# Optimization experiments

Hardware: AMD Instinct MI355X
Metric: run time of the kernel (lower is better)

## Reference

```python
import jax, jax.numpy as jnp
import numpy as np

B, S, C, HEADS = 1, 4096, 640, 8
AH, AW = 64, 64            # attn-resolution grid, AH*AW == S
MH, MW = 512, 512          # full-res mask size
NEG = -1e9                 # finite large negative (safe for fully-masked rows)


def nearest_resize(x, h, w):
    # torch F.interpolate(mode='nearest'): idx = floor(i * H_in / H_out)
    H, W = x.shape[-2], x.shape[-1]
    ri = (jnp.arange(h) * H) // h
    ci = (jnp.arange(w) * W) // w
    return x[..., ri, :][..., :, ci]


def sdpa(q, k, v, mask, heads):
    # q,k,v: [B,S,C]; mask: [B,1,S,S] bool (True = attend), broadcasts over heads
    b, s, c = q.shape
    d = c // heads
    qh = q.reshape(b, s, heads, d).transpose(0, 2, 1, 3)  # bhsd
    kh = k.reshape(b, s, heads, d).transpose(0, 2, 1, 3)
    vh = v.reshape(b, s, heads, d).transpose(0, 2, 1, 3)
    scores = jnp.einsum('bhqd,bhkd->bhqk', qh, kh) / jnp.sqrt(jnp.asarray(d, qh.dtype))
    scores = jnp.where(mask, scores, NEG)
    attn = jax.nn.softmax(scores, axis=-1)
    out = jnp.einsum('bhqk,bhkd->bhqd', attn, vh)
    return out.transpose(0, 2, 1, 3).reshape(b, s, c)


def setup_inputs():
    key = jax.random.key(0)
    ks = jax.random.split(key, 14)
    std = 1.0 / np.sqrt(C)
    w = lambda k: (jax.random.normal(k, (C, C), jnp.float32) * std)
    return {
        'hidden_states': jax.random.normal(ks[0], (B, S, C), jnp.float32),
        'mask': jax.random.randint(ks[1], (B, 1, MH, MW), 0, 4, jnp.int32),
        'inpainting_mask': jax.random.randint(ks[2], (B, 1, MH, MW), 0, 2, jnp.int32),
        'Wq': w(ks[3]), 'Wk': w(ks[4]), 'Wv': w(ks[5]),
        'Wq_ent': w(ks[6]), 'Wk_ent': w(ks[7]), 'Wv_ent': w(ks[8]),
        'Wq_out': w(ks[9]), 'Wk_out': w(ks[10]), 'Wv_out': w(ks[11]),
        'Wo': w(ks[12]),
    }


def reference(hidden_states, mask, inpainting_mask, Wq, Wk, Wv,
              Wq_ent, Wk_ent, Wv_ent, Wq_out, Wk_out, Wv_out, Wo):
    residual = hidden_states
    b, s, c = hidden_states.shape

    # --- interpolation-derived masks (kept as [B,1,S,S]; broadcasts over heads) ---
    m = nearest_resize(mask, AH, AW).reshape(b, 1, s)                 # entity labels
    attn_mask = m[:, :, :, None] == m[:, :, None, :]                  # same-entity [B,1,S,S]
    im = nearest_resize(inpainting_mask, AH, AW).reshape(b, 1, s)
    outside_key = (im[:, :, None, :] == 0)                            # [B,1,1,S]
    attn_mask_outside = attn_mask & outside_key                       # [B,1,S,S]

    # --- projections ---
    q = hidden_states @ Wq.T
    k = hidden_states @ Wk.T
    v = hidden_states @ Wv.T
    q_e = hidden_states @ Wq_ent.T
    k_e = hidden_states @ Wk_ent.T
    v_e = hidden_states @ Wv_ent.T
    q_o = hidden_states @ Wq_out.T
    k_o = hidden_states @ Wk_out.T
    v_o = hidden_states @ Wv_out.T

    # --- three SDPA branches ---
    hs_orig = sdpa(q, k, v, attn_mask, HEADS)            # original attention
    hs_ent = sdpa(q_e, k_e, v_e, attn_mask, 1)           # entity attention (1 head)
    hs_out = sdpa(q_o, k_o, v_o, attn_mask_outside, HEADS)  # outside attention

    hs = hs_orig + hs_ent + hs_out
    return hs @ Wo.T + residual
```

## Files before the change

kernel.cpp:

```cpp
#include <hip/hip_runtime.h>
#include <cstdint>

typedef __attribute__((ext_vector_type(8))) short bf16x8;
typedef __attribute__((ext_vector_type(4))) short bf16x4;
typedef __attribute__((ext_vector_type(4))) float f32x4;

#define S_LEN 4096
#define CDIM  640
#define NPROJ 5760

__device__ __forceinline__ f32x4 mfma16(bf16x4 a, bf16x4 b, f32x4 c){
#if defined(__HIP_DEVICE_COMPILE__) && __HIP_DEVICE_COMPILE__
  return __builtin_amdgcn_mfma_f32_16x16x16bf16_1k(a, b, c, 0, 0, 0);
#else
  (void)a; (void)b;
  return c;
#endif
}

__device__ __forceinline__ void gload_lds(const unsigned short* g, unsigned short* l){
#if defined(__HIP_DEVICE_COMPILE__) && __HIP_DEVICE_COMPILE__
  __builtin_amdgcn_global_load_lds((const __attribute__((address_space(1))) unsigned int*)g,
                                   (__attribute__((address_space(3))) unsigned int*)l, 16, 0, 0);
#else
  (void)g; (void)l;
#endif
}

__device__ __forceinline__ unsigned short f2bf(float f){
  union { float f; uint32_t u; } v; v.f = f;
  uint32_t u = v.u;
  return (unsigned short)((u + 0x7fffu + ((u >> 16) & 1u)) >> 16);
}
__device__ __forceinline__ float b2f(unsigned short h){
  union { uint32_t u; float f; } v; v.u = ((uint32_t)h) << 16;
  return v.f;
}

__global__ void k_labels(const int* __restrict__ mask, const int* __restrict__ inp,
                         int* __restrict__ labels){
  int s = blockIdx.x * 256 + threadIdx.x;
  if (s >= S_LEN) return;
  int y = s >> 6, x = s & 63;
  int off = (y * 8) * 512 + x * 8;
  int m = mask[off] & 0xff;
  int o = (inp[off] == 0) ? 0x100 : 0;
  labels[s] = m | o;
}

__global__ void k_hist(const int* __restrict__ labels, int* __restrict__ boff, int* __restrict__ cnt){
  __shared__ int h[4];
  if (threadIdx.x < 4) h[threadIdx.x] = 0;
  __syncthreads();
  for (int s = threadIdx.x; s < S_LEN; s += 256) atomicAdd(&h[labels[s] & 3], 1);
  __syncthreads();
  if (threadIdx.x == 0){
    int a = 0;
    for (int c = 0; c < 4; c++){ boff[c] = a; a += h[c]; }
    boff[4] = a;
  }
  if (threadIdx.x < 4) cnt[threadIdx.x] = 0;
}

__global__ void k_perm(const int* __restrict__ labels, const int* __restrict__ boff,
                       int* __restrict__ cnt, int* __restrict__ perm,
                       int* __restrict__ inv, int* __restrict__ labP){
  int s = blockIdx.x * 256 + threadIdx.x;
  if (s >= S_LEN) return;
  int lab = labels[s];
  int c = lab & 3;
  int pos = boff[c] + atomicAdd(&cnt[c], 1);
  perm[pos] = s; inv[s] = pos; labP[pos] = lab;
}

__global__ void k_tiles(const int* __restrict__ labP, const int* __restrict__ boff,
                        int4* __restrict__ qtinfo, float* __restrict__ rowsum){
  int t = threadIdx.x;
  __shared__ int nkt[32];
  if (t < 32){
    int c0 = labP[t * 128] & 3, c1 = labP[t * 128 + 127] & 3;
    int lo = boff[c0] & ~127, hi = (boff[c1 + 1] + 127) & ~127;
    qtinfo[t].x = lo; qtinfo[t].y = hi; qtinfo[t].w = 0;
    nkt[t] = (hi - lo) >> 7;
  }
  __syncthreads();
  if (t == 0){
    int a = 0;
    for (int i = 0; i < 32; i++){ qtinfo[i].z = a; a += nkt[i]; }
  }
  for (int s = t; s < S_LEN; s += 256) rowsum[s] = 0.f;
}

__global__ void k_cvt_hs(const float* __restrict__ src, unsigned short* __restrict__ dst, int n){
  int idx = (blockIdx.x * 256 + threadIdx.x) * 4;
  if (idx >= n) return;
  float4 v = *(const float4*)(src + idx);
  ushort4 o;
  o.x = f2bf(v.x); o.y = f2bf(v.y); o.z = f2bf(v.z); o.w = f2bf(v.w);
  *(ushort4*)(dst + idx) = o;
}

struct WPtrs { const float* w[10]; };

__global__ void k_cvt_w(WPtrs p, unsigned short* __restrict__ dst){
  int e = (blockIdx.x * 256 + threadIdx.x) * 4;
  if (e >= 10 * 409600) return;
  int a = e / 409600, r = e % 409600;
  float sc = (a == 0 || a == 6) ? 0.11180339887498948f
           : (a == 3 ? 0.03952847075210474f : 1.0f);
  float4 v = *(const float4*)(p.w[a] + r);
  ushort4 o;
  o.x = f2bf(v.x * sc); o.y = f2bf(v.y * sc); o.z = f2bf(v.z * sc); o.w = f2bf(v.w * sc);
  *(ushort4*)(dst + e) = o;
}

template<int EPI>
__global__ __launch_bounds__(256) void k_gemm(const unsigned short* __restrict__ A,
                                              const unsigned short* __restrict__ B,
                                              int M, int N, int K, int ldc,
                                              const int* __restrict__ rowmap,
                                              unsigned short* __restrict__ Cb,
                                              float* __restrict__ Cf,
                                              const float* __restrict__ resid){
  __shared__ __align__(16) unsigned short As[128 * 32];
  __shared__ __align__(16) unsigned short Bs[128 * 32];
  int m0 = blockIdx.y * 128, n0 = blockIdx.x * 128;
  int tid = threadIdx.x;
  int wid = tid >> 6, lane = tid & 63;
  int quad = lane >> 4, l16 = lane & 15;
  int wm = (wid >> 1) * 64, wn = (wid & 1) * 64;
  f32x4 acc[4][4];
#pragma unroll
  for (int i = 0; i < 4; i++)
#pragma unroll
    for (int j = 0; j < 4; j++) acc[i][j] = f32x4{0.f, 0.f, 0.f, 0.f};

  for (int k0 = 0; k0 < K; k0 += 32){
    __syncthreads();
#pragma unroll
    for (int u = 0; u < 2; u++){
      int c = tid + u * 256;
      int row = c >> 2, off = (c & 3) * 8;
      gload_lds(&A[(size_t)(m0 + row) * K + k0 + off], &As[c * 8]);
      gload_lds(&B[(size_t)(n0 + row) * K + k0 + off], &Bs[c * 8]);
    }
    __syncthreads();
    bf16x8 af[4], bfr[4];
#pragma unroll
    for (int t = 0; t < 4; t++){
      af[t]  = *(const bf16x8*)(&As[(wm + t * 16 + l16) * 32 + quad * 8]);
      bfr[t] = *(const bf16x8*)(&Bs[(wn + t * 16 + l16) * 32 + quad * 8]);
    }
#pragma unroll
    for (int mt = 0; mt < 4; mt++)
#pragma unroll
      for (int nt = 0; nt < 4; nt++)
        acc[mt][nt] = __builtin_amdgcn_mfma_f32_16x16x32_bf16(af[mt], bfr[nt], acc[mt][nt], 0, 0, 0);
  }
#pragma unroll
  for (int mt = 0; mt < 4; mt++)
#pragma unroll
    for (int nt = 0; nt < 4; nt++)
#pragma unroll
      for (int r = 0; r < 4; r++){
        int row = m0 + wm + mt * 16 + quad * 4 + r;
        int col = n0 + wn + nt * 16 + l16;
        float v = acc[mt][nt][r];
        if (EPI == 0){
          Cb[(size_t)rowmap[row] * ldc + col] = f2bf(v);
        } else {
          int ro = rowmap[row];
          Cf[(size_t)ro * ldc + col] = v + resid[(size_t)ro * ldc + col];
        }
      }
}

__global__ void k_transpose_v(const unsigned short* __restrict__ proj, unsigned short* __restrict__ vT){
  __shared__ unsigned short T[64][65];
  int z = blockIdx.z;
  int s0 = blockIdx.x * 64, c0 = blockIdx.y * 64;
  int colbase = 1280 + z * 1920 + c0;
  unsigned short* dst = vT + (size_t)z * CDIM * S_LEN;
  int tid = threadIdx.x;
  for (int i = tid; i < 64 * 64; i += 256){
    int r = i >> 6, c = i & 63;
    T[r][c] = proj[(size_t)(s0 + r) * NPROJ + colbase + c];
  }
  __syncthreads();
  for (int i = tid; i < 64 * 64; i += 256){
    int c = i >> 6, r = i & 63;
    dst[(size_t)(c0 + c) * S_LEN + s0 + r] = T[r][c];
  }
}

#define KP 84
#define VP 76
__global__ __launch_bounds__(256, 2) void k_attn80(const unsigned short* __restrict__ proj,
                                                   const unsigned short* __restrict__ vT,
                                                   const int* __restrict__ labP,
                                                   const int4* __restrict__ qtinfo,
                                                   unsigned short* __restrict__ outP){
  __shared__ __align__(16) unsigned short Ks[64 * KP];
  __shared__ __align__(16) unsigned short Vt[80 * VP];
  __shared__ __align__(16) int labk[64];
  int tid = threadIdx.x, wid = tid >> 6, lane = tid & 63;
  int quad = lane >> 4, l16 = lane & 15;
  int q0 = blockIdx.x * 128;
  int h  = blockIdx.y;
  bool OUTSIDE = (blockIdx.z == 1);
  int qc = (OUTSIDE ? 3840 : 0) + h * 80;
  int kc = (OUTSIDE ? 4480 : 640) + h * 80;
  const unsigned short* vTb = vT + (size_t)(OUTSIDE ? 2 : 0) * CDIM * S_LEN;
  int4 qi = qtinfo[blockIdx.x];
  int t0 = qi.x >> 6, t1 = qi.y >> 6;

  int qrow0 = q0 + wid * 32 + l16;
  int qrow1 = qrow0 + 16;
  bf16x4 qf0[5], qf1[5];
#pragma unroll
  for (int dc = 0; dc < 5; dc++){
    qf0[dc] = *(const bf16x4*)&proj[(size_t)qrow0 * NPROJ + qc + dc * 16 + quad * 4];
    qf1[dc] = *(const bf16x4*)&proj[(size_t)qrow1 * NPROJ + qc + dc * 16 + quad * 4];
  }
  int lq0 = labP[qrow0] & 0xff, lq1 = labP[qrow1] & 0xff;

  float lp0 = 0.f, lp1 = 0.f;
  f32x4 Oc0[5], Oc1[5];
#pragma unroll
  for (int t = 0; t < 5; t++){ Oc0[t] = f32x4{0.f,0.f,0.f,0.f}; Oc1[t] = f32x4{0.f,0.f,0.f,0.f}; }

  for (int kt = t0; kt < t1; kt++){
    int key0 = kt * 64;
    __syncthreads();
#pragma unroll
    for (int u = 0; u < 3; u++){
      int c = tid + u * 256;
      if (c < 640){
        int krow = c / 10, koff = (c % 10) * 8;
        int vrow = c >> 3, voff = (c & 7) * 8;
        *(uint4*)&Ks[krow * KP + koff] =
          *(const uint4*)&proj[(size_t)(key0 + krow) * NPROJ + kc + koff];
        *(uint4*)&Vt[vrow * VP + voff] =
          *(const uint4*)&vTb[(size_t)(h * 80 + vrow) * S_LEN + key0 + voff];
      }
    }
    if (tid < 64) labk[tid] = labP[key0 + tid];
    __syncthreads();

#pragma unroll
    for (int kg = 0; kg < 4; kg++){
      f32x4 sa0 = f32x4{0.f,0.f,0.f,0.f}, sa1 = f32x4{0.f,0.f,0.f,0.f};
#pragma unroll
      for (int dc = 0; dc < 5; dc++){
        bf16x4 kf = *(const bf16x4*)&Ks[(kg * 16 + l16) * KP + dc * 16 + quad * 4];
        sa0 = mfma16(kf, qf0[dc], sa0);
        sa1 = mfma16(kf, qf1[dc], sa1);
      }
      int4 lk4 = *(const int4*)&labk[kg * 16 + quad * 4];
      bool m0 = !OUTSIDE || (lk4.x & 0x100), m1 = !OUTSIDE || (lk4.y & 0x100);
      bool m2 = !OUTSIDE || (lk4.z & 0x100), m3 = !OUTSIDE || (lk4.w & 0x100);
      int k0l = lk4.x & 0xff, k1l = lk4.y & 0xff, k2l = lk4.z & 0xff, k3l = lk4.w & 0xff;
      bf16x4 pf0, pf1;
      {
        float p0 = (k0l == lq0 && m0) ? __expf(sa0[0]) : 0.f;
        float p1 = (k1l == lq0 && m1) ? __expf(sa0[1]) : 0.f;
        float p2 = (k2l == lq0 && m2) ? __expf(sa0[2]) : 0.f;
        float p3 = (k3l == lq0 && m3) ? __expf(sa0[3]) : 0.f;
        lp0 += (p0 + p1) + (p2 + p3);
        pf0[0] = (short)f2bf(p0); pf0[1] = (short)f2bf(p1);
        pf0[2] = (short)f2bf(p2); pf0[3] = (short)f2bf(p3);
      }
      {
        float p0 = (k0l == lq1 && m0) ? __expf(sa1[0]) : 0.f;
        float p1 = (k1l == lq1 && m1) ? __expf(sa1[1]) : 0.f;
        float p2 = (k2l == lq1 && m2) ? __expf(sa1[2]) : 0.f;
        float p3 = (k3l == lq1 && m3) ? __expf(sa1[3]) : 0.f;
        lp1 += (p0 + p1) + (p2 + p3);
        pf1[0] = (short)f2bf(p0); pf1[1] = (short)f2bf(p1);
        pf1[2] = (short)f2bf(p2); pf1[3] = (short)f2bf(p3);
      }
#pragma unroll
      for (int dt = 0; dt < 5; dt++){
        bf16x4 vf = *(const bf16x4*)&Vt[(dt * 16 + l16) * VP + kg * 16 + quad * 4];
        Oc0[dt] = mfma16(vf, pf0, Oc0[dt]);
        Oc1[dt] = mfma16(vf, pf1, Oc1[dt]);
      }
    }
  }
  lp0 += __shfl_xor(lp0, 16); lp0 += __shfl_xor(lp0, 32);
  lp1 += __shfl_xor(lp1, 16); lp1 += __shfl_xor(lp1, 32);
  float iL0 = 1.f / lp0, iL1 = 1.f / lp1;
  unsigned short* dst = outP + (size_t)blockIdx.z * S_LEN * CDIM;
#pragma unroll
  for (int dt = 0; dt < 5; dt++){
    ushort4 o;
    o.x = f2bf(Oc0[dt][0] * iL0); o.y = f2bf(Oc0[dt][1] * iL0);
    o.z = f2bf(Oc0[dt][2] * iL0); o.w = f2bf(Oc0[dt][3] * iL0);
    *(ushort4*)&dst[(size_t)qrow0 * CDIM + h * 80 + dt * 16 + quad * 4] = o;
    o.x = f2bf(Oc1[dt][0] * iL1); o.y = f2bf(Oc1[dt][1] * iL1);
    o.z = f2bf(Oc1[dt][2] * iL1); o.w = f2bf(Oc1[dt][3] * iL1);
    *(ushort4*)&dst[(size_t)qrow1 * CDIM + h * 80 + dt * 16 + quad * 4] = o;
  }
}

__global__ __launch_bounds__(256) void k_ent_qk(const unsigned short* __restrict__ proj,
                                                const int* __restrict__ labP,
                                                const int4* __restrict__ qtinfo,
                                                unsigned short* __restrict__ Sbuf,
                                                float* __restrict__ rowsum){
  int qt = blockIdx.y;
  int4 qi = qtinfo[qt];
  int nkt = (qi.y - qi.x) >> 7;
  if ((int)blockIdx.x >= nkt) return;
  int m0 = qt * 128, n0 = qi.x + blockIdx.x * 128;
  __shared__ __align__(16) unsigned short As[128 * 32];
  __shared__ __align__(16) unsigned short Bs[128 * 32];
  __shared__ int lQ[128], lK[128];
  int tid = threadIdx.x, wid = tid >> 6, lane = tid & 63;
  int quad = lane >> 4, l16 = lane & 15;
  int wm = (wid >> 1) * 64, wn = (wid & 1) * 64;
  if (tid < 128) lQ[tid] = labP[m0 + tid] & 0xff;
  else           lK[tid - 128] = labP[n0 + tid - 128] & 0xff;
  f32x4 acc[4][4];
#pragma unroll
  for (int i = 0; i < 4; i++)
#pragma unroll
    for (int j = 0; j < 4; j++) acc[i][j] = f32x4{0.f, 0.f, 0.f, 0.f};

  for (int k0 = 0; k0 < 640; k0 += 32){
    __syncthreads();
#pragma unroll
    for (int u = 0; u < 2; u++){
      int c = tid + u * 256;
      int row = c >> 2, off = (c & 3) * 8;
      gload_lds(&proj[(size_t)(m0 + row) * NPROJ + 1920 + k0 + off], &As[c * 8]);
      gload_lds(&proj[(size_t)(n0 + row) * NPROJ + 2560 + k0 + off], &Bs[c * 8]);
    }
    __syncthreads();
    bf16x8 af[4], bfr[4];
#pragma unroll
    for (int t = 0; t < 4; t++){
      af[t]  = *(const bf16x8*)(&As[(wm + t * 16 + l16) * 32 + quad * 8]);
      bfr[t] = *(const bf16x8*)(&Bs[(wn + t * 16 + l16) * 32 + quad * 8]);
    }
#pragma unroll
    for (int mt = 0; mt < 4; mt++)
#pragma unroll
      for (int nt = 0; nt < 4; nt++)
        acc[mt][nt] = __builtin_amdgcn_mfma_f32_16x16x32_bf16(af[mt], bfr[nt], acc[mt][nt], 0, 0, 0);
  }
  unsigned short* St = Sbuf + ((size_t)(qi.z + blockIdx.x)) * 16384;
#pragma unroll
  for (int mt = 0; mt < 4; mt++)
#pragma unroll
    for (int r = 0; r < 4; r++){
      int lrow = wm + mt * 16 + quad * 4 + r;
      int myq = lQ[lrow];
      float psum = 0.f;
#pragma unroll
      for (int nt = 0; nt < 4; nt++){
        int lcol = wn + nt * 16 + l16;
        float p = (myq == lK[lcol]) ? __expf(acc[mt][nt][r]) : 0.f;
        St[lrow * 128 + lcol] = f2bf(p);
        psum += p;
      }
#pragma unroll
      for (int m = 1; m < 16; m <<= 1) psum += __shfl_xor(psum, m);
      if (l16 == 0) atomicAdd(&rowsum[m0 + lrow], psum);
    }
}

__global__ __launch_bounds__(256) void k_ent_pv(const unsigned short* __restrict__ Sbuf,
                                                const unsigned short* __restrict__ veT,
                                                const int4* __restrict__ qtinfo,
                                                const float* __restrict__ rowsum,
                                                const unsigned short* __restrict__ planes,
                                                unsigned short* __restrict__ attnS){
  int qt = blockIdx.y, d0 = blockIdx.x * 128;
  int4 qi = qtinfo[qt];
  int m0 = qt * 128;
  int nk = qi.y - qi.x;
  __shared__ __align__(16) unsigned short As[128 * 32];
  __shared__ __align__(16) unsigned short Bs[128 * 32];
  int tid = threadIdx.x, wid = tid >> 6, lane = tid & 63;
  int quad = lane >> 4, l16 = lane & 15;
  int wm = (wid >> 1) * 64, wn = (wid & 1) * 64;
  f32x4 acc[4][4];
#pragma unroll
  for (int i = 0; i < 4; i++)
#pragma unroll
    for (int j = 0; j < 4; j++) acc[i][j] = f32x4{0.f, 0.f, 0.f, 0.f};

  for (int kk = 0; kk < nk; kk += 32){
    const unsigned short* St = Sbuf + ((size_t)(qi.z + (kk >> 7))) * 16384;
    int kloc = kk & 127;
    __syncthreads();
#pragma unroll
    for (int u = 0; u < 2; u++){
      int c = tid + u * 256;
      int row = c >> 2, off = (c & 3) * 8;
      gload_lds(&St[row * 128 + kloc + off], &As[c * 8]);
      gload_lds(&veT[(size_t)(d0 + row) * S_LEN + qi.x + kk + off], &Bs[c * 8]);
    }
    __syncthreads();
    bf16x8 af[4], bfr[4];
#pragma unroll
    for (int t = 0; t < 4; t++){
      af[t]  = *(const bf16x8*)(&As[(wm + t * 16 + l16) * 32 + quad * 8]);
      bfr[t] = *(const bf16x8*)(&Bs[(wn + t * 16 + l16) * 32 + quad * 8]);
    }
#pragma unroll
    for (int mt = 0; mt < 4; mt++)
#pragma unroll
      for (int nt = 0; nt < 4; nt++)
        acc[mt][nt] = __builtin_amdgcn_mfma_f32_16x16x32_bf16(af[mt], bfr[nt], acc[mt][nt], 0, 0, 0);
  }
#pragma unroll
  for (int mt = 0; mt < 4; mt++)
#pragma unroll
    for (int r = 0; r < 4; r++){
      int row = m0 + wm + mt * 16 + quad * 4 + r;
      float invL = 1.f / rowsum[row];
#pragma unroll
      for (int nt = 0; nt < 4; nt++){
        int col = d0 + wn + nt * 16 + l16;
        size_t idx = (size_t)row * CDIM + col;
        float v = acc[mt][nt][r] * invL + b2f(planes[idx]) + b2f(planes[(size_t)S_LEN * CDIM + idx]);
        attnS[idx] = f2bf(v);
      }
    }
}

extern "C" void kernel_launch(void* const* d_in, const int* in_sizes, int n_in,
                              void* d_out, int out_size, void* d_ws, size_t ws_size,
                              hipStream_t stream){
  const float* hs  = (const float*)d_in[0];
  const int* mask  = (const int*)d_in[1];
  const int* inp   = (const int*)d_in[2];
  char* ws = (char*)d_ws;
  int*            labels  = (int*)(ws + 0);
  int*            boff    = (int*)(ws + 16384);
  int*            cnt     = (int*)(ws + 16640);
  int*            perm    = (int*)(ws + 16896);
  int*            inv     = (int*)(ws + 33280);
  int*            labP    = (int*)(ws + 49664);
  int4*           qtinfo  = (int4*)(ws + 66560);
  float*          rowsum  = (float*)(ws + 67072);
  unsigned short* hsb     = (unsigned short*)(ws + 131072);
  unsigned short* Wall    = (unsigned short*)(ws + 5373952);
  unsigned short* proj    = (unsigned short*)(ws + 13565952);
  unsigned short* vT      = (unsigned short*)(ws + 60751872);
  unsigned short* planes  = (unsigned short*)(ws + 76480512);
  unsigned short* Sbuf    = (unsigned short*)(ws + 86966272);
  unsigned short* attnS   = (unsigned short*)(ws + 120520704);
  unsigned short* Wob     = Wall + 9 * 409600;

  k_labels<<<16, 256, 0, stream>>>(mask, inp, labels);
  k_hist<<<1, 256, 0, stream>>>(labels, boff, cnt);
  k_perm<<<16, 256, 0, stream>>>(labels, boff, cnt, perm, inv, labP);
  k_tiles<<<1, 256, 0, stream>>>(labP, boff, qtinfo, rowsum);
  k_cvt_hs<<<(S_LEN * CDIM / 4 + 255) / 256, 256, 0, stream>>>(hs, hsb, S_LEN * CDIM);
  WPtrs wp;
  for (int i = 0; i < 10; i++) wp.w[i] = (const float*)d_in[3 + i];
  k_cvt_w<<<(10 * 409600 / 4 + 255) / 256, 256, 0, stream>>>(wp, Wall);

  k_gemm<0><<<dim3(45, 32), 256, 0, stream>>>(hsb, Wall, S_LEN, NPROJ, CDIM, NPROJ,
                                              inv, proj, nullptr, nullptr);
  k_transpose_v<<<dim3(64, 10, 3), 256, 0, stream>>>(proj, vT);

  k_attn80<<<dim3(32, 8, 2), 256, 0, stream>>>(proj, vT, labP, qtinfo, planes);

  k_ent_qk<<<dim3(32, 32), 256, 0, stream>>>(proj, labP, qtinfo, Sbuf, rowsum);
  k_ent_pv<<<dim3(5, 32), 256, 0, stream>>>(Sbuf, vT + (size_t)1 * CDIM * S_LEN,
                                            qtinfo, rowsum, planes, attnS);

  k_gemm<1><<<dim3(5, 32), 256, 0, stream>>>(attnS, Wob, S_LEN, CDIM, CDIM, CDIM,
                                             perm, nullptr, (float*)d_out, hs);
}
```

Before: 410.1 us.

## Double-buffer K/V tiles with register prefetch in attention kernel

The attention kernel now keeps two LDS buffers for the K, V and label tiles and prefetches the tile after next into registers, so global loads overlap with the MFMA work on the current tile. Each iteration writes the already-loaded tile into the spare buffer and then issues the next global loads. This drops one of the two barriers per iteration. In exchange, LDS use roughly doubles and register pressure rises, which may hurt the two-blocks-per-CU occupancy target.

```diff
diff --git a/kernel.cpp b/kernel.cpp
--- a/kernel.cpp
+++ b/kernel.cpp
@@ -200,9 +200,9 @@
                                                    const int* __restrict__ labP,
                                                    const int4* __restrict__ qtinfo,
                                                    unsigned short* __restrict__ outP){
-  __shared__ __align__(16) unsigned short Ks[64 * KP];
-  __shared__ __align__(16) unsigned short Vt[80 * VP];
-  __shared__ __align__(16) int labk[64];
+  __shared__ __align__(16) unsigned short Ks[2][64 * KP];
+  __shared__ __align__(16) unsigned short Vt[2][80 * VP];
+  __shared__ __align__(16) int labk[2][64];
   int tid = threadIdx.x, wid = tid >> 6, lane = tid & 63;
   int quad = lane >> 4, l16 = lane & 15;
   int q0 = blockIdx.x * 128;
@@ -229,34 +229,59 @@
 #pragma unroll
   for (int t = 0; t < 5; t++){ Oc0[t] = f32x4{0.f,0.f,0.f,0.f}; Oc1[t] = f32x4{0.f,0.f,0.f,0.f}; }
 
-  for (int kt = t0; kt < t1; kt++){
-    int key0 = kt * 64;
-    __syncthreads();
+  uint4 kreg[3], vreg[3];
+  int lreg = 0;
+  auto LOADT = [&](int kt_){
+    int key0 = kt_ * 64;
 #pragma unroll
     for (int u = 0; u < 3; u++){
       int c = tid + u * 256;
       if (c < 640){
         int krow = c / 10, koff = (c % 10) * 8;
         int vrow = c >> 3, voff = (c & 7) * 8;
-        *(uint4*)&Ks[krow * KP + koff] =
-          *(const uint4*)&proj[(size_t)(key0 + krow) * NPROJ + kc + koff];
-        *(uint4*)&Vt[vrow * VP + voff] =
-          *(const uint4*)&vTb[(size_t)(h * 80 + vrow) * S_LEN + key0 + voff];
-      }
-    }
-    if (tid < 64) labk[tid] = labP[key0 + tid];
-    __syncthreads();
+        kreg[u] = *(const uint4*)&proj[(size_t)(key0 + krow) * NPROJ + kc + koff];
+        vreg[u] = *(const uint4*)&vTb[(size_t)(h * 80 + vrow) * S_LEN + key0 + voff];
+      }
+    }
+    if (tid < 64) lreg = labP[key0 + tid];
+  };
+  auto WRITET = [&](int b){
+#pragma unroll
+    for (int u = 0; u < 3; u++){
+      int c = tid + u * 256;
+      if (c < 640){
+        int krow = c / 10, koff = (c % 10) * 8;
+        int vrow = c >> 3, voff = (c & 7) * 8;
+        *(uint4*)&Ks[b][krow * KP + koff] = kreg[u];
+        *(uint4*)&Vt[b][vrow * VP + voff] = vreg[u];
+      }
+    }
+    if (tid < 64) labk[b][tid] = lreg;
+  };
+
+  LOADT(t0);
+  WRITET(0);
+  if (t0 + 1 < t1) LOADT(t0 + 1);
+  __syncthreads();
+
+  int cur = 0;
+  for (int kt = t0; kt < t1; kt++){
+    int nxt = cur ^ 1;
+    if (kt + 1 < t1){
+      WRITET(nxt);
+      if (kt + 2 < t1) LOADT(kt + 2);
+    }
 
 #pragma unroll
     for (int kg = 0; kg < 4; kg++){
       f32x4 sa0 = f32x4{0.f,0.f,0.f,0.f}, sa1 = f32x4{0.f,0.f,0.f,0.f};
 #pragma unroll
       for (int dc = 0; dc < 5; dc++){
-        bf16x4 kf = *(const bf16x4*)&Ks[(kg * 16 + l16) * KP + dc * 16 + quad * 4];
+        bf16x4 kf = *(const bf16x4*)&Ks[cur][(kg * 16 + l16) * KP + dc * 16 + quad * 4];
         sa0 = mfma16(kf, qf0[dc], sa0);
         sa1 = mfma16(kf, qf1[dc], sa1);
       }
-      int4 lk4 = *(const int4*)&labk[kg * 16 + quad * 4];
+      int4 lk4 = *(const int4*)&labk[cur][kg * 16 + quad * 4];
       bool m0 = !OUTSIDE || (lk4.x & 0x100), m1 = !OUTSIDE || (lk4.y & 0x100);
       bool m2 = !OUTSIDE || (lk4.z & 0x100), m3 = !OUTSIDE || (lk4.w & 0x100);
       int k0l = lk4.x & 0xff, k1l = lk4.y & 0xff, k2l = lk4.z & 0xff, k3l = lk4.w & 0xff;
@@ -281,11 +306,13 @@
       }
 #pragma unroll
       for (int dt = 0; dt < 5; dt++){
-        bf16x4 vf = *(const bf16x4*)&Vt[(dt * 16 + l16) * VP + kg * 16 + quad * 4];
+        bf16x4 vf = *(const bf16x4*)&Vt[cur][(dt * 16 + l16) * VP + kg * 16 + quad * 4];
         Oc0[dt] = mfma16(vf, pf0, Oc0[dt]);
         Oc1[dt] = mfma16(vf, pf1, Oc1[dt]);
       }
     }
+    __syncthreads();
+    cur = nxt;
   }
   lp0 += __shfl_xor(lp0, 16); lp0 += __shfl_xor(lp0, 32);
   lp1 += __shfl_xor(lp1, 16); lp1 += __shfl_xor(lp1, 32);
```

Measured after the change: 457.2 us. 11.5% more time.
